# Optimization experiments

Hardware: AMD Instinct MI355X
Metric: run time of the kernel (lower is better)

Reference implementation:

```python
import jax, jax.numpy as jnp
import numpy as np

B, P, ENC = 128, 196, 512
H = 512   # must equal ENC (gate * awe elementwise in original)
E = 512   # embed size
A = 512   # attention dim
V = 32000
L = 20    # caption length; decode steps T = L - 1


def setup_inputs() -> dict:
    key = jax.random.key(0)
    ks = jax.random.split(key, 24)
    s = 0.02
    features = jax.random.normal(ks[0], (B, P, ENC), jnp.float32)
    captions = jax.random.randint(ks[1], (B, L), 0, V)
    # lengths sorted descending (pack_padded_sequence contract); force max = L
    len_np = np.sort(np.array(jax.random.randint(ks[2], (B,), 2, L + 1)))[::-1].copy()
    len_np[0] = L
    lengths = jnp.asarray(len_np, jnp.int32)
    rn = lambda k, sh: jax.random.normal(k, sh, jnp.float32) * s
    return {
        "features": features, "captions": captions, "lengths": lengths,
        "w_enc_att": rn(ks[3], (A, ENC)), "b_enc_att": rn(ks[4], (A,)),
        "w_dec_att": rn(ks[5], (A, H)), "b_dec_att": rn(ks[6], (A,)),
        "w_full": rn(ks[7], (A,)), "b_full": rn(ks[8], (1,)),
        "embed_w": rn(ks[9], (V, E)),
        "w_ih": rn(ks[10], (4 * H, E + ENC)), "b_ih": rn(ks[11], (4 * H,)),
        "w_hh": rn(ks[12], (4 * H, H)), "b_hh": rn(ks[13], (4 * H,)),
        "w_init_h": rn(ks[14], (H, ENC)), "b_init_h": rn(ks[15], (H,)),
        "w_init_c": rn(ks[16], (H, ENC)), "b_init_c": rn(ks[17], (H,)),
        "w_beta": rn(ks[18], (H, ENC)), "b_beta": rn(ks[19], (H,)),
        "w_fc": rn(ks[20], (V, H)), "b_fc": rn(ks[21], (V,)),
    }


def _decode(features, captions, lengths, w_enc_att, b_enc_att, w_dec_att,
            b_dec_att, w_full, b_full, embed_w, w_ih, b_ih, w_hh, b_hh,
            w_init_h, b_init_h, w_init_c, b_init_c, w_beta, b_beta, w_fc, b_fc):
    T = captions.shape[1] - 1  # static max decode length
    dec_len = lengths - 1      # [B]
    emb = embed_w[captions]    # [B, L, E]
    fmean = features.mean(axis=1)                       # [B, ENC]
    h0 = fmean @ w_init_h.T + b_init_h                  # [B, H]
    c0 = fmean @ w_init_c.T + b_init_c
    att1 = features @ w_enc_att.T + b_enc_att           # [B, P, A] (precomputed, step-invariant)

    xs_emb = jnp.swapaxes(emb[:, :T, :], 0, 1)          # [T, B, E]
    active = jnp.arange(T)[:, None] < dec_len[None, :]  # [T, B], mimics batch_size_t slicing

    def step(carry, xs):
        h, c = carry
        x_t, act = xs                                   # [B,E], [B]
        m = act[:, None]
        # additive attention
        att2 = h @ w_dec_att.T + b_dec_att              # [B, A]
        e = jnp.einsum('bpa,a->bp', jax.nn.relu(att1 + att2[:, None, :]), w_full) + b_full[0]
        alpha = jax.nn.softmax(e, axis=1)               # [B, P]
        awe = jnp.einsum('bp,bpe->be', alpha, features) # [B, ENC]
        gate = jax.nn.sigmoid(h @ w_beta.T + b_beta)    # [B, H] (H == ENC)
        awe = gate * awe
        # LSTMCell (torch gate order i, f, g, o)
        z = jnp.concatenate([x_t, awe], axis=1)         # [B, E+ENC]
        gates = z @ w_ih.T + b_ih + h @ w_hh.T + b_hh   # [B, 4H]
        i_g, f_g, g_g, o_g = jnp.split(gates, 4, axis=1)
        c_new = jax.nn.sigmoid(f_g) * c + jax.nn.sigmoid(i_g) * jnp.tanh(g_g)
        h_new = jax.nn.sigmoid(o_g) * jnp.tanh(c_new)
        # inactive rows keep old state (torch only updates h[:batch_size_t])
        h2 = jnp.where(m, h_new, h)
        c2 = jnp.where(m, c_new, c)
        preds = h_new @ w_fc.T + b_fc                   # dropout in eval mode (identity)
        preds = jnp.where(m, preds, 0.0)
        alpha_o = jnp.where(m, alpha, 0.0)
        return (h2, c2), (preds, alpha_o)

    (_, _), (preds_t, alphas_t) = jax.lax.scan(step, (h0, c0), (xs_emb, active))
    predictions = jnp.swapaxes(preds_t, 0, 1)           # [B, T, V]
    alphas = jnp.swapaxes(alphas_t, 0, 1)               # [B, T, P]
    return predictions, alphas


def reference(features, captions, lengths, w_enc_att, b_enc_att, w_dec_att,
              b_dec_att, w_full, b_full, embed_w, w_ih, b_ih, w_hh, b_hh,
              w_init_h, b_init_h, w_init_c, b_init_c, w_beta, b_beta, w_fc, b_fc):
    return _decode(features, captions, lengths, w_enc_att, b_enc_att, w_dec_att,
                   b_dec_att, w_full, b_full, embed_w, w_ih, b_ih, w_hh, b_hh,
                   w_init_h, b_init_h, w_init_c, b_init_c, w_beta, b_beta,
                   w_fc, b_fc)
```

## Files before the change

### kernel.cpp

```cpp
#include <hip/hip_runtime.h>
#include <hip/hip_bf16.h>

typedef __attribute__((ext_vector_type(8))) short short8;
typedef __attribute__((ext_vector_type(4))) float floatx4;

#define NB 128
#define NP 196
#define NH 512
#define NV 32000
#define NT 19

__device__ __forceinline__ float bf2f(short s) {
  unsigned int u = ((unsigned int)(unsigned short)s) << 16;
  return __builtin_bit_cast(float, u);
}
__device__ __forceinline__ short f2bf(float f) {
  unsigned int u = __builtin_bit_cast(unsigned int, f);
  unsigned int lsb = (u >> 16) & 1u;
  u += 0x7fffu + lsb;
  return (short)(u >> 16);
}
__device__ __forceinline__ float sigf(float x) { return 1.f / (1.f + expf(-x)); }
__device__ __forceinline__ float ldw(int fl, const void* p, int i) {
  return fl ? bf2f(((const short*)p)[i]) : ((const float*)p)[i];
}

__global__ void k_detect(const unsigned int* __restrict__ w, int* __restrict__ flagp) {
  __shared__ int cnt;
  if (threadIdx.x == 0) cnt = 0;
  __syncthreads();
  int local = 0;
  for (int i = threadIdx.x; i < 4096; i += 256) {
    unsigned int lo = w[i] & 0xFFFFu;
    unsigned int ex = (lo >> 7) & 0xFFu;
    if (ex >= 110u && ex <= 135u) local++;
  }
  atomicAdd(&cnt, local);
  __syncthreads();
  if (threadIdx.x == 0) *flagp = (cnt > 2048) ? 1 : 0;
}

__global__ void k_convall(const void* __restrict__ s0, const void* __restrict__ s1,
                          const void* __restrict__ s2, const void* __restrict__ s3,
                          const void* __restrict__ s4, const void* __restrict__ s5,
                          const void* __restrict__ s6, const void* __restrict__ s7,
                          const void* __restrict__ s8, const void* __restrict__ s9,
                          short* __restrict__ dst, const int* __restrict__ flagp) {
  int fl = *flagp;
  const int totc = 50069504 / 8;
  for (int c = blockIdx.x * 256 + threadIdx.x; c < totc; c += gridDim.x * 256) {
    int i = c * 8;
    const void* src;
    int off;
    if (i < 12845056)      { src = s0; off = i; }
    else if (i < 29229056) { src = s1; off = i - 12845056; }
    else if (i < 45613056) { src = s2; off = i - 29229056; }
    else if (i < 47710208) { src = s3; off = i - 45613056; }
    else if (i < 48758784) { src = s4; off = i - 47710208; }
    else if (i < 49020928) { src = s5; off = i - 48758784; }
    else if (i < 49283072) { src = s6; off = i - 49020928; }
    else if (i < 49545216) { src = s7; off = i - 49283072; }
    else if (i < 49807360) { src = s8; off = i - 49545216; }
    else                   { src = s9; off = i - 49807360; }
    if (fl) {
      ((short8*)dst)[c] = *(const short8*)((const short*)src + off);
    } else {
      const float* sp = (const float*)src + off;
      short8 o;
#pragma unroll
      for (int j = 0; j < 8; ++j) o[j] = f2bf(sp[j]);
      ((short8*)dst)[c] = o;
    }
  }
}

__global__ void k_fmean(const short* __restrict__ feat, short* __restrict__ fmean) {
  int b = blockIdx.x;
  for (int e = threadIdx.x; e < NH; e += 256) {
    float s = 0.f;
    const short* fp = feat + (size_t)b * (NP * NH) + e;
    for (int p = 0; p < NP; ++p) s += bf2f(fp[p * NH]);
    fmean[b * NH + e] = f2bf(s * (1.f / 196.f));
  }
}

__global__ void k_init(const short* __restrict__ fmean,
                       const short* __restrict__ w_init_h, const void* __restrict__ b_init_h,
                       const short* __restrict__ w_init_c, const void* __restrict__ b_init_c,
                       short* __restrict__ hbuf, float* __restrict__ cbuf,
                       const int* __restrict__ flagp) {
  int fl = *flagp;
  int wave = threadIdx.x >> 6, lane = threadIdx.x & 63;
  int rlo = lane & 15, quad = lane >> 4;
  int n = (blockIdx.x * 4 + wave) * 16 + rlo;
  const short* brow = (n < 512 ? w_init_h + (size_t)n * 512 : w_init_c + (size_t)(n - 512) * 512) + quad * 8;
  const short* arow = fmean + rlo * 512 + quad * 8;
  floatx4 acc[8];
#pragma unroll
  for (int mt = 0; mt < 8; ++mt) acc[mt] = (floatx4){0.f, 0.f, 0.f, 0.f};
  for (int k = 0; k < 512; k += 32) {
    short8 bfr = *(const short8*)(brow + k);
#pragma unroll
    for (int mt = 0; mt < 8; ++mt) {
      short8 afr = *(const short8*)(arow + mt * (16 * 512) + k);
      acc[mt] = __builtin_amdgcn_mfma_f32_16x16x32_bf16(afr, bfr, acc[mt], 0, 0, 0);
    }
  }
  float bias = (n < 512) ? ldw(fl, b_init_h, n) : ldw(fl, b_init_c, n - 512);
#pragma unroll
  for (int mt = 0; mt < 8; ++mt)
#pragma unroll
    for (int r = 0; r < 4; ++r) {
      int bb = mt * 16 + quad * 4 + r;
      float v = acc[mt][r] + bias;
      if (n < 512) hbuf[bb * 512 + n] = f2bf(v);
      else cbuf[bb * 512 + (n - 512)] = v;
    }
}

__global__ void k_att1(const short* __restrict__ feat, const short* __restrict__ w_enc,
                       const void* __restrict__ b_enc, short* __restrict__ att1,
                       const int* __restrict__ flagp) {
  int fl = *flagp;
  int wave = threadIdx.x >> 6, lane = threadIdx.x & 63;
  int rlo = lane & 15, quad = lane >> 4;
  int n = (blockIdx.x * 4 + wave) * 16 + rlo;
  int mbase = blockIdx.y * 128;
  const short* brow = w_enc + (size_t)n * 512 + quad * 8;
  const short* arow = feat + (size_t)(mbase + rlo) * 512 + quad * 8;
  floatx4 acc[8];
#pragma unroll
  for (int mt = 0; mt < 8; ++mt) acc[mt] = (floatx4){0.f, 0.f, 0.f, 0.f};
  for (int k = 0; k < 512; k += 32) {
    short8 bfr = *(const short8*)(brow + k);
#pragma unroll
    for (int mt = 0; mt < 8; ++mt) {
      short8 afr = *(const short8*)(arow + (size_t)mt * (16 * 512) + k);
      acc[mt] = __builtin_amdgcn_mfma_f32_16x16x32_bf16(afr, bfr, acc[mt], 0, 0, 0);
    }
  }
  float bias = ldw(fl, b_enc, n);
#pragma unroll
  for (int mt = 0; mt < 8; ++mt)
#pragma unroll
    for (int r = 0; r < 4; ++r) {
      int m = mbase + mt * 16 + quad * 4 + r;
      att1[(size_t)m * 512 + n] = f2bf(acc[mt][r] + bias);
    }
}

__global__ void k_xpart(const int* __restrict__ captions, const short* __restrict__ embed_w,
                        const short* __restrict__ w_ih, const void* __restrict__ b_ih,
                        const void* __restrict__ b_hh, float* __restrict__ xp,
                        const int* __restrict__ flagp) {
  int fl = *flagp;
  int wave = threadIdx.x >> 6, lane = threadIdx.x & 63;
  int rlo = lane & 15, quad = lane >> 4;
  int t = blockIdx.y;
  int n = (blockIdx.x * 4 + wave) * 16 + rlo;
  const short* brow = w_ih + (size_t)n * 1024 + quad * 8;
  int tok[8];
#pragma unroll
  for (int mt = 0; mt < 8; ++mt) tok[mt] = captions[(mt * 16 + rlo) * 20 + t];
  floatx4 acc[8];
#pragma unroll
  for (int mt = 0; mt < 8; ++mt) acc[mt] = (floatx4){0.f, 0.f, 0.f, 0.f};
  for (int k = 0; k < 512; k += 32) {
    short8 bfr = *(const short8*)(brow + k);
#pragma unroll
    for (int mt = 0; mt < 8; ++mt) {
      short8 afr = *(const short8*)(embed_w + (size_t)tok[mt] * 512 + quad * 8 + k);
      acc[mt] = __builtin_amdgcn_mfma_f32_16x16x32_bf16(afr, bfr, acc[mt], 0, 0, 0);
    }
  }
  float bias = ldw(fl, b_ih, n) + ldw(fl, b_hh, n);
#pragma unroll
  for (int mt = 0; mt < 8; ++mt)
#pragma unroll
    for (int r = 0; r < 4; ++r) {
      int bb = mt * 16 + quad * 4 + r;
      xp[((size_t)t * 128 + bb) * 2048 + n] = acc[mt][r] + bias;
    }
}

__global__ void k_hproj(const short* __restrict__ hbuf,
                        const short* __restrict__ w_dec, const void* __restrict__ b_dec,
                        const short* __restrict__ w_beta, const void* __restrict__ b_beta,
                        const short* __restrict__ w_hh, float* __restrict__ abuf,
                        const int* __restrict__ flagp) {
  int fl = *flagp;
  int wave = threadIdx.x >> 6, lane = threadIdx.x & 63;
  int rlo = lane & 15, quad = lane >> 4;
  int n = (blockIdx.x * 4 + wave) * 16 + rlo;
  const short* brow;
  float bias;
  if (n < 512)       { brow = w_dec  + (size_t)n * 512;          bias = ldw(fl, b_dec, n); }
  else if (n < 1024) { brow = w_beta + (size_t)(n - 512) * 512;  bias = ldw(fl, b_beta, n - 512); }
  else               { brow = w_hh   + (size_t)(n - 1024) * 512; bias = 0.f; }
  brow += quad * 8;
  const short* arow = hbuf + rlo * 512 + quad * 8;
  floatx4 acc[8];
#pragma unroll
  for (int mt = 0; mt < 8; ++mt) acc[mt] = (floatx4){0.f, 0.f, 0.f, 0.f};
  for (int k = 0; k < 512; k += 32) {
    short8 bfr = *(const short8*)(brow + k);
#pragma unroll
    for (int mt = 0; mt < 8; ++mt) {
      short8 afr = *(const short8*)(arow + mt * (16 * 512) + k);
      acc[mt] = __builtin_amdgcn_mfma_f32_16x16x32_bf16(afr, bfr, acc[mt], 0, 0, 0);
    }
  }
#pragma unroll
  for (int mt = 0; mt < 8; ++mt)
#pragma unroll
    for (int r = 0; r < 4; ++r) {
      int bb = mt * 16 + quad * 4 + r;
      abuf[(size_t)bb * 3072 + n] = acc[mt][r] + bias;
    }
}

__global__ void k_score(const short* __restrict__ att1, const float* __restrict__ abuf,
                        const void* __restrict__ w_full, float* __restrict__ escore,
                        const int* __restrict__ flagp) {
  int fl = *flagp;
  int wave = threadIdx.x >> 6, lane = threadIdx.x & 63;
  int gw = blockIdx.x * 4 + wave;
  int r0 = gw * 8;
  float wfr[8];
#pragma unroll
  for (int j = 0; j < 8; ++j) wfr[j] = ldw(fl, w_full, lane * 8 + j);
#pragma unroll
  for (int rr = 0; rr < 8; ++rr) {
    int r = r0 + rr;
    int b = r / 196;
    const float* a2 = abuf + (size_t)b * 3072 + lane * 8;
    floatx4 a2a = *(const floatx4*)a2;
    floatx4 a2b = *(const floatx4*)(a2 + 4);
    short8 v = *(const short8*)(att1 + (size_t)r * 512 + lane * 8);
    float s = 0.f;
    s += fmaxf(bf2f(v[0]) + a2a[0], 0.f) * wfr[0];
    s += fmaxf(bf2f(v[1]) + a2a[1], 0.f) * wfr[1];
    s += fmaxf(bf2f(v[2]) + a2a[2], 0.f) * wfr[2];
    s += fmaxf(bf2f(v[3]) + a2a[3], 0.f) * wfr[3];
    s += fmaxf(bf2f(v[4]) + a2b[0], 0.f) * wfr[4];
    s += fmaxf(bf2f(v[5]) + a2b[1], 0.f) * wfr[5];
    s += fmaxf(bf2f(v[6]) + a2b[2], 0.f) * wfr[6];
    s += fmaxf(bf2f(v[7]) + a2b[3], 0.f) * wfr[7];
#pragma unroll
    for (int off = 32; off >= 1; off >>= 1) s += __shfl_xor(s, off, 64);
    if (lane == 0) escore[r] = s;
  }
}

__global__ void k_ctx(const float* __restrict__ escore, const short* __restrict__ feat,
                      const float* __restrict__ abuf, const int* __restrict__ lengths,
                      short* __restrict__ awe, void* __restrict__ d_out,
                      const int* __restrict__ flagp, int t) {
  int fl = *flagp;
  int ec = blockIdx.x;
  int b = blockIdx.y;
  int tid = threadIdx.x, wave = tid >> 6, lane = tid & 63;
  __shared__ float sm[196];
  __shared__ float psum[4][128];
  for (int p = tid; p < NP; p += 256) sm[p] = escore[b * NP + p];
  __syncthreads();
  bool act = t < (lengths[b] - 1);
  if (wave == 0) {
    float v0 = sm[lane], v1 = sm[lane + 64], v2 = sm[lane + 128];
    float v3 = (lane < 4) ? sm[lane + 192] : -1e30f;
    float m = fmaxf(fmaxf(v0, v1), fmaxf(v2, v3));
#pragma unroll
    for (int off = 32; off >= 1; off >>= 1) m = fmaxf(m, __shfl_xor(m, off, 64));
    float e0 = expf(v0 - m), e1 = expf(v1 - m), e2 = expf(v2 - m);
    float e3 = (lane < 4) ? expf(v3 - m) : 0.f;
    float s = e0 + e1 + e2 + e3;
#pragma unroll
    for (int off = 32; off >= 1; off >>= 1) s += __shfl_xor(s, off, 64);
    float inv = 1.f / s;
    float a0 = e0 * inv, a1 = e1 * inv, a2 = e2 * inv, a3 = e3 * inv;
    sm[lane] = a0; sm[lane + 64] = a1; sm[lane + 128] = a2;
    if (lane < 4) sm[lane + 192] = a3;
    if (ec == 0) {
      size_t ob = (size_t)NB * NT * NV + ((size_t)b * NT + t) * NP;
      float o0 = act ? a0 : 0.f, o1 = act ? a1 : 0.f, o2 = act ? a2 : 0.f, o3 = act ? a3 : 0.f;
      if (fl) {
        short* op = (short*)d_out;
        op[ob + lane] = f2bf(o0); op[ob + lane + 64] = f2bf(o1); op[ob + lane + 128] = f2bf(o2);
        if (lane < 4) op[ob + lane + 192] = f2bf(o3);
      } else {
        float* op = (float*)d_out;
        op[ob + lane] = o0; op[ob + lane + 64] = o1; op[ob + lane + 128] = o2;
        if (lane < 4) op[ob + lane + 192] = o3;
      }
    }
  }
  __syncthreads();
  int eoff = ec * 128 + lane * 2;
  const short* fb = feat + (size_t)b * (NP * NH) + eoff;
  float acc0 = 0.f, acc1 = 0.f;
  for (int p = wave; p < NP; p += 4) {
    unsigned int u = *(const unsigned int*)(fb + (size_t)p * NH);
    float al = sm[p];
    acc0 = fmaf(al, __builtin_bit_cast(float, u << 16), acc0);
    acc1 = fmaf(al, __builtin_bit_cast(float, u & 0xFFFF0000u), acc1);
  }
  psum[wave][lane * 2] = acc0;
  psum[wave][lane * 2 + 1] = acc1;
  __syncthreads();
  if (tid < 128) {
    int e = ec * 128 + tid;
    float s = psum[0][tid] + psum[1][tid] + psum[2][tid] + psum[3][tid];
    float gate = sigf(abuf[(size_t)b * 3072 + 512 + e]);
    awe[b * NH + e] = f2bf(gate * s);
  }
}

__global__ void k_gates_lstm(const short* __restrict__ awe_bf, const short* __restrict__ w_ih,
                             const float* __restrict__ xp, const float* __restrict__ abuf,
                             const int* __restrict__ lengths, float* __restrict__ cbuf,
                             short* __restrict__ hbuf, short* __restrict__ hnall, int t) {
  int tid = threadIdx.x, wave = tid >> 6, lane = tid & 63;
  int rlo = lane & 15, quad = lane >> 4;
  int n = wave * 512 + blockIdx.x * 16 + rlo;
  const short* brow = w_ih + (size_t)n * 1024 + 512 + quad * 8;
  const short* arow = awe_bf + rlo * 512 + quad * 8;
  floatx4 acc[8];
#pragma unroll
  for (int mt = 0; mt < 8; ++mt) acc[mt] = (floatx4){0.f, 0.f, 0.f, 0.f};
  for (int k = 0; k < 512; k += 32) {
    short8 bfr = *(const short8*)(brow + k);
#pragma unroll
    for (int mt = 0; mt < 8; ++mt) {
      short8 afr = *(const short8*)(arow + mt * (16 * 512) + k);
      acc[mt] = __builtin_amdgcn_mfma_f32_16x16x32_bf16(afr, bfr, acc[mt], 0, 0, 0);
    }
  }
  __shared__ float gsm[4][128][17];
#pragma unroll
  for (int mt = 0; mt < 8; ++mt)
#pragma unroll
    for (int r = 0; r < 4; ++r) {
      int bb = mt * 16 + quad * 4 + r;
      float v = acc[mt][r] + xp[((size_t)t * 128 + bb) * 2048 + n] + abuf[(size_t)bb * 3072 + 1024 + n];
      gsm[wave][bb][rlo] = v;
    }
  __syncthreads();
  for (int idx = tid; idx < 2048; idx += 256) {
    int bb = idx >> 4, jl = idx & 15;
    int j = blockIdx.x * 16 + jl;
    float ig = gsm[0][bb][jl], fg = gsm[1][bb][jl], gg = gsm[2][bb][jl], og = gsm[3][bb][jl];
    float co = cbuf[bb * 512 + j];
    float cn = sigf(fg) * co + sigf(ig) * tanhf(gg);
    float hn = sigf(og) * tanhf(cn);
    hnall[(size_t)t * (128 * 512) + bb * 512 + j] = f2bf(hn);
    if (t < lengths[bb] - 1) {
      cbuf[bb * 512 + j] = cn;
      hbuf[bb * 512 + j] = f2bf(hn);
    }
  }
}

__global__ void __launch_bounds__(256, 2)
k_preds_all(const short* __restrict__ hnall, const short* __restrict__ w_fc,
            const void* __restrict__ b_fc, const int* __restrict__ lengths,
            void* __restrict__ d_out, const int* __restrict__ flagp) {
  int fl = *flagp;
  int tid = threadIdx.x, wave = tid >> 6, lane = tid & 63;
  int rlo = lane & 15, quad = lane >> 4;
  int n0 = blockIdx.x * 64;
  int mw = wave * 32;
  __shared__ short Bl[64 * 512];

#pragma unroll
  for (int j = 0; j < 16; ++j) {
    int idx = j * 256 + tid;
    int row = idx >> 6, c8 = idx & 63;
    int sw = (c8 * 16) ^ ((row & 7) << 4);
    short8 vb = *(const short8*)(w_fc + (size_t)(n0 + row) * 512 + c8 * 8);
    *(short8*)((char*)Bl + row * 1024 + sw) = vb;
  }
  __syncthreads();

  float bias[4];
  int lenr[2][4];
#pragma unroll
  for (int nf = 0; nf < 4; ++nf) bias[nf] = ldw(fl, b_fc, n0 + nf * 16 + rlo);
#pragma unroll
  for (int mt = 0; mt < 2; ++mt)
#pragma unroll
    for (int r = 0; r < 4; ++r) lenr[mt][r] = lengths[mw + mt * 16 + quad * 4 + r];

  for (int t = 0; t < NT; ++t) {
    floatx4 acc[2][4];
#pragma unroll
    for (int mt = 0; mt < 2; ++mt)
#pragma unroll
      for (int nf = 0; nf < 4; ++nf) acc[mt][nf] = (floatx4){0.f, 0.f, 0.f, 0.f};
    const short* abase = hnall + (size_t)t * (128 * 512);
#pragma unroll
    for (int ks = 0; ks < 16; ++ks) {
      short8 afr[2], bfr[4];
#pragma unroll
      for (int mt = 0; mt < 2; ++mt)
        afr[mt] = *(const short8*)(abase + (size_t)(mw + mt * 16 + rlo) * 512 + ks * 32 + quad * 8);
#pragma unroll
      for (int nf = 0; nf < 4; ++nf) {
        int row = nf * 16 + rlo;
        bfr[nf] = *(const short8*)((const char*)Bl + row * 1024 +
                                   ((ks * 64 + quad * 16) ^ ((row & 7) << 4)));
      }
#pragma unroll
      for (int mt = 0; mt < 2; ++mt)
#pragma unroll
        for (int nf = 0; nf < 4; ++nf)
          acc[mt][nf] = __builtin_amdgcn_mfma_f32_16x16x32_bf16(afr[mt], bfr[nf], acc[mt][nf], 0, 0, 0);
    }
#pragma unroll
    for (int mt = 0; mt < 2; ++mt)
#pragma unroll
      for (int r = 0; r < 4; ++r) {
        int bb = mw + mt * 16 + quad * 4 + r;
        bool act = t < lenr[mt][r] - 1;
#pragma unroll
        for (int nf = 0; nf < 4; ++nf) {
          int n = n0 + nf * 16 + rlo;
          float v = act ? (acc[mt][nf][r] + bias[nf]) : 0.f;
          size_t oi = ((size_t)bb * NT + t) * NV + n;
          if (fl) __builtin_nontemporal_store(f2bf(v), &((short*)d_out)[oi]);
          else __builtin_nontemporal_store(v, &((float*)d_out)[oi]);
        }
      }
  }
}

extern "C" void kernel_launch(void* const* d_in, const int* in_sizes, int n_in,
                              void* d_out, int out_size, void* d_ws, size_t ws_size,
                              hipStream_t stream) {
  const void* features = d_in[0];
  const int* captions = (const int*)d_in[1];
  const int* lengths = (const int*)d_in[2];
  const void* w_enc_att = d_in[3];
  const void* b_enc_att = d_in[4];
  const void* w_dec_att = d_in[5];
  const void* b_dec_att = d_in[6];
  const void* w_full = d_in[7];
  const void* embed_w = d_in[9];
  const void* w_ih = d_in[10];
  const void* b_ih = d_in[11];
  const void* w_hh = d_in[12];
  const void* b_hh = d_in[13];
  const void* w_init_h = d_in[14];
  const void* b_init_h = d_in[15];
  const void* w_init_c = d_in[16];
  const void* b_init_c = d_in[17];
  const void* w_beta = d_in[18];
  const void* b_beta = d_in[19];
  const void* w_fc = d_in[20];
  const void* b_fc = d_in[21];

  char* ws = (char*)d_ws;
  int* flagp = (int*)ws; ws += 16;
  short* cfeat = (short*)ws; ws += (size_t)12845056 * 2;
  short* cembed = (short*)ws; ws += (size_t)16384000 * 2;
  short* cwfc = (short*)ws; ws += (size_t)16384000 * 2;
  short* cwih = (short*)ws; ws += (size_t)2097152 * 2;
  short* cwhh = (short*)ws; ws += (size_t)1048576 * 2;
  short* cwenc = (short*)ws; ws += (size_t)262144 * 2;
  short* cwdec = (short*)ws; ws += (size_t)262144 * 2;
  short* cwbeta = (short*)ws; ws += (size_t)262144 * 2;
  short* cwinith = (short*)ws; ws += (size_t)262144 * 2;
  short* cwinitc = (short*)ws; ws += (size_t)262144 * 2;
  short* att1 = (short*)ws; ws += (size_t)25088 * 512 * 2;
  float* xp   = (float*)ws; ws += (size_t)2432 * 2048 * 4;
  float* abuf = (float*)ws; ws += (size_t)128 * 3072 * 4;
  float* escore = (float*)ws; ws += (size_t)25088 * 4;
  short* hbuf = (short*)ws; ws += 128 * 512 * 2;
  short* hnall = (short*)ws; ws += (size_t)NT * 128 * 512 * 2;
  short* awe  = (short*)ws; ws += 128 * 512 * 2;
  short* fmean = (short*)ws; ws += 128 * 512 * 2;
  float* cbuf = (float*)ws; ws += 128 * 512 * 4;

  k_detect<<<1, 256, 0, stream>>>((const unsigned int*)features, flagp);
  k_convall<<<2048, 256, 0, stream>>>(features, embed_w, w_fc, w_ih, w_hh,
                                      w_enc_att, w_dec_att, w_beta, w_init_h, w_init_c,
                                      cfeat, flagp);

  k_fmean<<<128, 256, 0, stream>>>(cfeat, fmean);
  k_att1<<<dim3(8, 196), 256, 0, stream>>>(cfeat, cwenc, b_enc_att, att1, flagp);
  k_xpart<<<dim3(32, NT), 256, 0, stream>>>(captions, cembed, cwih, b_ih, b_hh, xp, flagp);
  k_init<<<16, 256, 0, stream>>>(fmean, cwinith, b_init_h, cwinitc, b_init_c, hbuf, cbuf, flagp);

  for (int t = 0; t < NT; ++t) {
    k_hproj<<<48, 256, 0, stream>>>(hbuf, cwdec, b_dec_att, cwbeta, b_beta, cwhh, abuf, flagp);
    k_score<<<784, 256, 0, stream>>>(att1, abuf, w_full, escore, flagp);
    k_ctx<<<dim3(4, 128), 256, 0, stream>>>(escore, cfeat, abuf, lengths, awe, d_out, flagp, t);
    k_gates_lstm<<<32, 256, 0, stream>>>(awe, cwih, xp, abuf, lengths, cbuf, hbuf, hnall, t);
  }
  k_preds_all<<<500, 256, 0, stream>>>(hnall, cwfc, b_fc, lengths, d_out, flagp);
}
```

Baseline: 2.336 ms.

## Retile hidden-state buffer for coalesced A loads and vectorize prediction stores via LDS

The per-step hidden state buffer is written in a k-blocked layout ([t][k/8][b][8]), so the vocab projection kernel can prefetch all A fragments for a timestep into registers with contiguous loads. The output epilogue now stages accumulator tiles through a shared-memory scratch buffer and writes four contiguous values per lane instead of scattered scalar stores. This targets the cost of uncoalesced writes to the large prediction tensor. In exchange it adds block-wide barriers inside the timestep loop, more LDS use and heavy register pressure from the 32 short8 prefetch registers.

```diff
diff --git a/kernel.cpp b/kernel.cpp
--- a/kernel.cpp
+++ b/kernel.cpp
@@ -2,6 +2,7 @@
 #include <hip/hip_bf16.h>
 
 typedef __attribute__((ext_vector_type(8))) short short8;
+typedef __attribute__((ext_vector_type(4))) short short4v;
 typedef __attribute__((ext_vector_type(4))) float floatx4;
 
 #define NB 128
@@ -352,7 +353,7 @@
     float co = cbuf[bb * 512 + j];
     float cn = sigf(fg) * co + sigf(ig) * tanhf(gg);
     float hn = sigf(og) * tanhf(cn);
-    hnall[(size_t)t * (128 * 512) + bb * 512 + j] = f2bf(hn);
+    hnall[(size_t)t * 65536 + (j >> 3) * 1024 + bb * 8 + (j & 7)] = f2bf(hn);
     if (t < lengths[bb] - 1) {
       cbuf[bb * 512 + j] = cn;
       hbuf[bb * 512 + j] = f2bf(hn);
@@ -370,6 +371,7 @@
   int n0 = blockIdx.x * 64;
   int mw = wave * 32;
   __shared__ short Bl[64 * 512];
+  __shared__ float scr[4][16][64];
 
 #pragma unroll
   for (int j = 0; j < 16; ++j) {
@@ -391,18 +393,23 @@
     for (int r = 0; r < 4; ++r) lenr[mt][r] = lengths[mw + mt * 16 + quad * 4 + r];
 
   for (int t = 0; t < NT; ++t) {
+    const short* abase = hnall + (size_t)t * 65536 + quad * 1024;
+    short8 areg[2][16];
+#pragma unroll
+    for (int mt = 0; mt < 2; ++mt)
+#pragma unroll
+      for (int ks = 0; ks < 16; ++ks)
+        areg[mt][ks] = *(const short8*)(abase + ks * 4096 + (mw + mt * 16 + rlo) * 8);
+
     floatx4 acc[2][4];
 #pragma unroll
     for (int mt = 0; mt < 2; ++mt)
 #pragma unroll
       for (int nf = 0; nf < 4; ++nf) acc[mt][nf] = (floatx4){0.f, 0.f, 0.f, 0.f};
-    const short* abase = hnall + (size_t)t * (128 * 512);
+
 #pragma unroll
     for (int ks = 0; ks < 16; ++ks) {
-      short8 afr[2], bfr[4];
-#pragma unroll
-      for (int mt = 0; mt < 2; ++mt)
-        afr[mt] = *(const short8*)(abase + (size_t)(mw + mt * 16 + rlo) * 512 + ks * 32 + quad * 8);
+      short8 bfr[4];
 #pragma unroll
       for (int nf = 0; nf < 4; ++nf) {
         int row = nf * 16 + rlo;
@@ -413,23 +420,36 @@
       for (int mt = 0; mt < 2; ++mt)
 #pragma unroll
         for (int nf = 0; nf < 4; ++nf)
-          acc[mt][nf] = __builtin_amdgcn_mfma_f32_16x16x32_bf16(afr[mt], bfr[nf], acc[mt][nf], 0, 0, 0);
-    }
-#pragma unroll
-    for (int mt = 0; mt < 2; ++mt)
-#pragma unroll
-      for (int r = 0; r < 4; ++r) {
-        int bb = mw + mt * 16 + quad * 4 + r;
-        bool act = t < lenr[mt][r] - 1;
-#pragma unroll
-        for (int nf = 0; nf < 4; ++nf) {
-          int n = n0 + nf * 16 + rlo;
-          float v = act ? (acc[mt][nf][r] + bias[nf]) : 0.f;
-          size_t oi = ((size_t)bb * NT + t) * NV + n;
-          if (fl) __builtin_nontemporal_store(f2bf(v), &((short*)d_out)[oi]);
-          else __builtin_nontemporal_store(v, &((float*)d_out)[oi]);
+          acc[mt][nf] = __builtin_amdgcn_mfma_f32_16x16x32_bf16(areg[mt][ks], bfr[nf], acc[mt][nf], 0, 0, 0);
+    }
+
+#pragma unroll
+    for (int mt = 0; mt < 2; ++mt) {
+#pragma unroll
+      for (int nf = 0; nf < 4; ++nf)
+#pragma unroll
+        for (int r = 0; r < 4; ++r) {
+          bool act = t < lenr[mt][r] - 1;
+          scr[wave][quad * 4 + r][nf * 16 + rlo] = act ? (acc[mt][nf][r] + bias[nf]) : 0.f;
+        }
+      __syncthreads();
+#pragma unroll
+      for (int g = 0; g < 4; ++g) {
+        int rowl = g * 4 + (lane >> 4);
+        int col = (lane & 15) * 4;
+        floatx4 v = *(const floatx4*)&scr[wave][rowl][col];
+        int bb = mw + mt * 16 + rowl;
+        size_t oi = ((size_t)bb * NT + t) * NV + n0 + col;
+        if (fl) {
+          short4v o;
+          o[0] = f2bf(v[0]); o[1] = f2bf(v[1]); o[2] = f2bf(v[2]); o[3] = f2bf(v[3]);
+          __builtin_nontemporal_store(o, (short4v*)&((short*)d_out)[oi]);
+        } else {
+          __builtin_nontemporal_store(v, (floatx4*)&((float*)d_out)[oi]);
         }
       }
+      __syncthreads();
+    }
   }
 }
 
```

New measurement: 2.161 ms. 1.08x faster.
